# Kernel tuning notes

Measured on AMD Instinct MI355X. Metric: run time of the kernel, lower is better.

## Reference

```python
import jax, jax.numpy as jnp
import numpy as np

B, T, C = 2, 2048, 1024
H, D = 16, 64
F = 4096
EPS = 1e-5


def _layernorm(x, scale, shift):
    mean = jnp.mean(x, axis=-1, keepdims=True)
    var = jnp.mean((x - mean) ** 2, axis=-1, keepdims=True)  # unbiased=False
    return scale * (x - mean) * jax.lax.rsqrt(var + EPS) + shift


def setup_inputs() -> dict:
    key = jax.random.key(0)
    ks = jax.random.split(key, 16)
    s = lambda k, shape, fan_in: jax.random.normal(k, shape, jnp.float32) * (1.0 / np.sqrt(fan_in))
    return {
        "x": jax.random.normal(ks[0], (B, T, C), jnp.float32),
        # weights stored [in, out] so y = x @ W + b (same math as torch Linear)
        "Wq": s(ks[1], (C, H * D), C), "bq": jnp.zeros((H * D,), jnp.float32),
        "Wk": s(ks[2], (C, H * D), C), "bk": jnp.zeros((H * D,), jnp.float32),
        "Wv": s(ks[3], (C, H * D), C), "bv": jnp.zeros((H * D,), jnp.float32),
        "Wo": s(ks[4], (H * D, C), H * D), "bo": jnp.zeros((C,), jnp.float32),
        "W1": s(ks[5], (C, F), C), "b1": jnp.zeros((F,), jnp.float32),
        "W2": s(ks[6], (F, C), F), "b2": jnp.zeros((C,), jnp.float32),
        "ln1_scale": jnp.ones((C,), jnp.float32), "ln1_shift": jnp.zeros((C,), jnp.float32),
        "ln2_scale": jnp.ones((C,), jnp.float32), "ln2_shift": jnp.zeros((C,), jnp.float32),
    }


def reference(x, Wq, bq, Wk, bk, Wv, bv, Wo, bo, W1, b1, W2, b2,
              ln1_scale, ln1_shift, ln2_scale, ln2_shift):
    b, t, c = x.shape
    # --- attention sub-block ---
    h = _layernorm(x, ln1_scale, ln1_shift)
    q = (h @ Wq + bq).reshape(b, t, H, D)
    k = (h @ Wk + bk).reshape(b, t, H, D)
    v = (h @ Wv + bv).reshape(b, t, H, D)
    scores = jnp.einsum('bqhd,bkhd->bhqk', q, k)  # [B,H,T,T]
    causal = jnp.tril(jnp.ones((t, t), dtype=bool))
    scores = jnp.where(causal, scores, -jnp.inf)
    attn = jax.nn.softmax(scores / np.sqrt(D), axis=-1)
    ctx = jnp.einsum('bhqk,bkhd->bqhd', attn, v).reshape(b, t, H * D)
    x = x + (ctx @ Wo + bo)  # drop_rate=0 -> dropout is identity
    # --- MLP sub-block ---
    h = _layernorm(x, ln2_scale, ln2_shift)
    h = jax.nn.gelu(h @ W1 + b1, approximate=False)
    x = x + (h @ W2 + b2)
    return x
```

## Files before the change

kernel.cpp:

```cpp
#include <hip/hip_runtime.h>
#include <hip/hip_bf16.h>
#include <stdint.h>

#define B_ 2
#define T_ 2048
#define C_ 1024
#define H_ 16
#define D_ 64
#define F_ 4096
#define M_ (B_*T_)

typedef unsigned short ushort_t;
typedef __attribute__((ext_vector_type(8))) short short8;
typedef __attribute__((ext_vector_type(4))) float f32x4;

__device__ __forceinline__ float bf2f(ushort_t u) {
    union { unsigned u; float f; } c; c.u = ((unsigned)u) << 16; return c.f;
}
__device__ __forceinline__ ushort_t f2bf(float f) {
    union { float f; unsigned u; } c; c.f = f;
    unsigned u = c.u;
    unsigned r = (u + 0x7FFFu + ((u >> 16) & 1u)) >> 16;
    return (ushort_t)r;
}

__device__ __forceinline__ float fexp2(float x) { return __builtin_amdgcn_exp2f(x); }

__device__ __forceinline__ void async16(void* lds, const void* g) {
    __builtin_amdgcn_global_load_lds(
        (const __attribute__((address_space(1))) unsigned int*)(uintptr_t)g,
        (__attribute__((address_space(3))) unsigned int*)(uintptr_t)lds,
        16, 0, 0);
}

__global__ __launch_bounds__(256) void transpose_all_k(
    const float* __restrict__ Wq, const float* __restrict__ Wk,
    const float* __restrict__ Wv, const float* __restrict__ Wo,
    const float* __restrict__ W1, const float* __restrict__ W2,
    ushort_t* __restrict__ oq, ushort_t* __restrict__ ok,
    ushort_t* __restrict__ ov, ushort_t* __restrict__ oo,
    ushort_t* __restrict__ o1, ushort_t* __restrict__ o2) {
    __shared__ ushort_t tile[32][33];
    int id = blockIdx.x;
    const float* in; ushort_t* out; int R, Cc, bx, by;
    if (id < 4096) {
        int w = id >> 10, loc = id & 1023;
        in  = w == 0 ? Wq : w == 1 ? Wk : w == 2 ? Wv : Wo;
        out = w == 0 ? oq : w == 1 ? ok : w == 2 ? ov : oo;
        R = 1024; Cc = 1024; bx = loc & 31; by = loc >> 5;
    } else if (id < 8192) {
        int loc = id - 4096; in = W1; out = o1; R = 1024; Cc = 4096;
        bx = loc & 127; by = loc >> 7;
    } else {
        int loc = id - 8192; in = W2; out = o2; R = 4096; Cc = 1024;
        bx = loc & 31; by = loc >> 5;
    }
    int tx = threadIdx.x, ty = threadIdx.y;
    int x = bx * 32 + tx;
    int y0 = by * 32;
#pragma unroll
    for (int i = 0; i < 32; i += 8)
        tile[ty + i][tx] = f2bf(in[(size_t)(y0 + ty + i) * Cc + x]);
    __syncthreads();
    int x2 = y0 + tx;
    int y2 = bx * 32;
#pragma unroll
    for (int i = 0; i < 32; i += 8)
        out[(size_t)(y2 + ty + i) * R + x2] = tile[tx][ty + i];
}

__global__ __launch_bounds__(256) void ln_kernel(const float* __restrict__ xin,
                                                 const float* __restrict__ scale_p,
                                                 const float* __restrict__ shift_p,
                                                 ushort_t* __restrict__ out) {
    int row = blockIdx.x, t = threadIdx.x;
    int wv = t >> 6, lane = t & 63;
    const float* xr = xin + (size_t)row * 1024 + t * 4;
    float4 v = *(const float4*)xr;
    float f[4] = {v.x, v.y, v.z, v.w};
    float s = f[0] + f[1] + f[2] + f[3];
    float q = f[0]*f[0] + f[1]*f[1] + f[2]*f[2] + f[3]*f[3];
#pragma unroll
    for (int off = 1; off < 64; off <<= 1) {
        s += __shfl_xor(s, off, 64);
        q += __shfl_xor(q, off, 64);
    }
    __shared__ float sh_s[4], sh_q[4];
    if (lane == 0) { sh_s[wv] = s; sh_q[wv] = q; }
    __syncthreads();
    float S = sh_s[0] + sh_s[1] + sh_s[2] + sh_s[3];
    float Q = sh_q[0] + sh_q[1] + sh_q[2] + sh_q[3];
    float mean = S * (1.0f / 1024.0f);
    float var = Q * (1.0f / 1024.0f) - mean * mean;
    float rstd = rsqrtf(var + 1e-5f);
    float4 scv = *(const float4*)(scale_p + t * 4);
    float4 shv = *(const float4*)(shift_p + t * 4);
    ushort4 o;
    o.x = f2bf((f[0] - mean) * rstd * scv.x + shv.x);
    o.y = f2bf((f[1] - mean) * rstd * scv.y + shv.y);
    o.z = f2bf((f[2] - mean) * rstd * scv.z + shv.z);
    o.w = f2bf((f[3] - mean) * rstd * scv.w + shv.w);
    *(ushort4*)(out + (size_t)row * 1024 + t * 4) = o;
}

template <int MT, int EPI>
__global__ __launch_bounds__(256) void gemm_bt(const ushort_t* __restrict__ A,
                                               const ushort_t* __restrict__ Bt,
                                               const float* __restrict__ b0,
                                               const float* __restrict__ b1,
                                               const float* __restrict__ b2,
                                               const float* __restrict__ res,
                                               void* __restrict__ out0,
                                               void* __restrict__ out1,
                                               void* __restrict__ out2,
                                               int M, int N, int K) {
    __shared__ ushort_t As[32 * MT * 32];
    __shared__ ushort_t Bs[128 * 32];
    const int t = threadIdx.x;
    const int wv = t >> 6, lane = t & 63, lo = lane & 15, hi = lane >> 4;
    const int wr = wv >> 1, wc = wv & 1;
    const int mb = blockIdx.y, nb = blockIdx.x;

    f32x4 acc[MT][4];
#pragma unroll
    for (int i = 0; i < MT; ++i)
#pragma unroll
        for (int j = 0; j < 4; ++j) acc[i][j] = (f32x4){0.f, 0.f, 0.f, 0.f};

    for (int k0 = 0; k0 < K; k0 += 32) {
#pragma unroll
        for (int i = 0; i < MT / 2; ++i) {
            int c = i * 256 + t;
            int row = c >> 2, kc = c & 3;
            async16((char*)As + (size_t)(i * 256 + wv * 64) * 16,
                    A + (size_t)(mb * 32 * MT + row) * K + k0 + kc * 8);
        }
#pragma unroll
        for (int i = 0; i < 2; ++i) {
            int c = i * 256 + t;
            int row = c >> 2, kc = c & 3;
            async16((char*)Bs + (size_t)(i * 256 + wv * 64) * 16,
                    Bt + (size_t)(nb * 128 + row) * K + k0 + kc * 8);
        }
        __syncthreads();

        short8 af[MT], bfr[4];
#pragma unroll
        for (int mi = 0; mi < MT; ++mi)
            af[mi] = *(const short8*)(As + (wr * 16 * MT + mi * 16 + lo) * 32 + hi * 8);
#pragma unroll
        for (int ni = 0; ni < 4; ++ni)
            bfr[ni] = *(const short8*)(Bs + (wc * 64 + ni * 16 + lo) * 32 + hi * 8);
#pragma unroll
        for (int mi = 0; mi < MT; ++mi)
#pragma unroll
            for (int ni = 0; ni < 4; ++ni)
                acc[mi][ni] = __builtin_amdgcn_mfma_f32_16x16x32_bf16(
                    af[mi], bfr[ni], acc[mi][ni], 0, 0, 0);
        __syncthreads();
    }

#pragma unroll
    for (int ni = 0; ni < 4; ++ni) {
        int n = nb * 128 + wc * 64 + ni * 16 + lo;
        float bn;
        ushort_t* obf = nullptr;
        int coln = n, seg = 0;
        if (EPI == 3) {
            seg = n >> 10; coln = n & 1023;
            bn = (seg == 0 ? b0 : seg == 1 ? b1 : b2)[coln];
            obf = (ushort_t*)(seg == 0 ? out0 : out1);
        } else {
            bn = b0[n];
        }
#pragma unroll
        for (int mi = 0; mi < MT; ++mi) {
            if (EPI == 3 && seg == 2) {
                int m0 = mb * 32 * MT + wr * 16 * MT + mi * 16 + 4 * hi;
                ushort4 pk;
                pk.x = f2bf(acc[mi][ni][0] + bn);
                pk.y = f2bf(acc[mi][ni][1] + bn);
                pk.z = f2bf(acc[mi][ni][2] + bn);
                pk.w = f2bf(acc[mi][ni][3] + bn);
                *(ushort4*)((ushort_t*)out2 + (size_t)coln * M + m0) = pk;
            } else {
#pragma unroll
                for (int r = 0; r < 4; ++r) {
                    int m = mb * 32 * MT + wr * 16 * MT + mi * 16 + 4 * hi + r;
                    float v = acc[mi][ni][r] + bn;
                    if (EPI == 1) {
                        size_t idx = (size_t)m * N + n;
                        ((float*)out0)[idx] = v + res[idx];
                    } else if (EPI == 2) {
                        v = 0.5f * v * (1.0f + erff(v * 0.70710678118654752f));
                        ((ushort_t*)out0)[(size_t)m * N + n] = f2bf(v);
                    } else {
                        obf[(size_t)m * 1024 + coln] = f2bf(v);
                    }
                }
            }
        }
    }
}

__global__ __launch_bounds__(256) void attn_kernel(const ushort_t* __restrict__ q,
                                                   const ushort_t* __restrict__ k,
                                                   const ushort_t* __restrict__ vt,
                                                   ushort_t* __restrict__ ctx) {
    __shared__ ushort_t Ks[2][64 * 64];
    __shared__ ushort_t VTs[2][64 * 64];
    __shared__ ushort_t Ps[8][16 * 72];

    const int t = threadIdx.x;
    const int wv = t >> 6, lane = t & 63, lo = lane & 15, hi = lane >> 4;
    const int id = blockIdx.x;
    const int s = id >> 5;
    const int qb = (s < 8) ? s : 23 - s;
    const int bh = id & 31, b = bh >> 4, h = bh & 15;
    const int q0 = qb * 128;
    const size_t headoff = (size_t)h * 64;
    const size_t rowbase = (size_t)b * T_ * 1024;
    const ushort_t* vbase = vt + headoff * (size_t)M_ + (size_t)b * T_;

    short8 qf[2][2];
#pragma unroll
    for (int g = 0; g < 2; ++g) {
        const ushort_t* qp = q + rowbase + (size_t)(q0 + g * 64 + wv * 16 + lo) * 1024 + headoff;
        qf[g][0] = *(const short8*)(qp + hi * 8);
        qf[g][1] = *(const short8*)(qp + 32 + hi * 8);
    }

    float m_g[2], l_g[2];
    f32x4 o_acc[2][4];
#pragma unroll
    for (int g = 0; g < 2; ++g) {
        m_g[g] = -1e30f; l_g[g] = 0.f;
#pragma unroll
        for (int dt = 0; dt < 4; ++dt) o_acc[g][dt] = (f32x4){0.f, 0.f, 0.f, 0.f};
    }

    const int ktmax = 2 * qb + 1;
    const float SC = 0.18033688011112042f;
    const f32x4 NEG4 = (f32x4){-1e30f, -1e30f, -1e30f, -1e30f};

    auto stage = [&](int bb, int kt) {
        const int k0s = kt * 64;
#pragma unroll
        for (int i = 0; i < 2; ++i) {
            int c = i * 256 + t;
            int row = c >> 3, c8 = c & 7;
            int gsw = c8 ^ (row & 7);
            async16((char*)&Ks[bb][0] + (size_t)(i * 256 + wv * 64) * 16,
                    k + rowbase + (size_t)(k0s + row) * 1024 + headoff + gsw * 8);
            async16((char*)&VTs[bb][0] + (size_t)(i * 256 + wv * 64) * 16,
                    vbase + (size_t)row * M_ + k0s + gsw * 8);
        }
    };

    auto softmax_g = [&](f32x4* sacc, int gi) {
        float mx = -1e30f;
#pragma unroll
        for (int kt16 = 0; kt16 < 4; ++kt16)
#pragma unroll
            for (int r = 0; r < 4; ++r) mx = fmaxf(mx, sacc[kt16][r]);
        mx = fmaxf(mx, __shfl_xor(mx, 16, 64));
        mx = fmaxf(mx, __shfl_xor(mx, 32, 64));
        float mnew = fmaxf(m_g[gi], mx);
        float alpha = fexp2(m_g[gi] - mnew);
        m_g[gi] = mnew;
        ushort_t* Pw = Ps[wv * 2 + gi];
        float rs = 0.f;
#pragma unroll
        for (int kt16 = 0; kt16 < 4; ++kt16) {
#pragma unroll
            for (int r = 0; r < 4; ++r) {
                float p = fexp2(sacc[kt16][r] - mnew);
                rs += p;
                Pw[lo * 72 + kt16 * 16 + 4 * hi + r] = f2bf(p);
            }
        }
        rs += __shfl_xor(rs, 16, 64);
        rs += __shfl_xor(rs, 32, 64);
        l_g[gi] = l_g[gi] * alpha + rs;
#pragma unroll
        for (int r = 0; r < 4; ++r) {
            float ab = __shfl(alpha, 4 * hi + r, 64);
#pragma unroll
            for (int dt = 0; dt < 4; ++dt) o_acc[gi][dt][r] *= ab;
        }
    };

    stage(0, 0);
    for (int kt = 0; kt <= ktmax; ++kt) {
        const int bb = kt & 1;
        const int k0 = kt * 64;
        __syncthreads();
        if (kt < ktmax) stage(bb ^ 1, kt + 1);

        short8 pf[2][2];
        int any_g[2];
#pragma unroll
        for (int g = 0; g < 2; ++g) {
            const int qg0 = q0 + g * 64 + wv * 16;
            const int diff = qg0 - k0;
            any_g[g] = (diff >= 0);
            if (!any_g[g]) continue;
            const int cmax = diff >= 48 ? 3 : (diff >> 4);

            f32x4 sacc[4];
#pragma unroll
            for (int kt16 = 0; kt16 < 4; ++kt16) {
                if (kt16 <= cmax) {
                    int row = kt16 * 16 + lo, sw = row & 7;
                    short8 kf0 = *(const short8*)(&Ks[bb][0] + row * 64 + (hi ^ sw) * 8);
                    short8 kf1 = *(const short8*)(&Ks[bb][0] + row * 64 + ((4 + hi) ^ sw) * 8);
                    f32x4 z = (f32x4){0.f, 0.f, 0.f, 0.f};
                    z = __builtin_amdgcn_mfma_f32_16x16x32_bf16(kf0, qf[g][0], z, 0, 0, 0);
                    z = __builtin_amdgcn_mfma_f32_16x16x32_bf16(kf1, qf[g][1], z, 0, 0, 0);
#pragma unroll
                    for (int r = 0; r < 4; ++r) sacc[kt16][r] = z[r] * SC;
                } else {
                    sacc[kt16] = NEG4;
                }
            }
            if (diff < 64) {
                const int qrow = diff + lo;
#pragma unroll
                for (int r = 0; r < 4; ++r) {
                    int key = cmax * 16 + 4 * hi + r;
                    if (key > qrow) sacc[cmax][r] = -1e30f;
                }
            }

            softmax_g(sacc, g);

            pf[g][0] = *(const short8*)(Ps[wv * 2 + g] + lo * 72 + hi * 8);
            pf[g][1] = *(const short8*)(Ps[wv * 2 + g] + lo * 72 + 32 + hi * 8);
        }

#pragma unroll
        for (int dt = 0; dt < 4; ++dt) {
            int row = dt * 16 + lo, sw = row & 7;
            short8 vf0 = *(const short8*)(&VTs[bb][0] + row * 64 + (hi ^ sw) * 8);
            short8 vf1 = *(const short8*)(&VTs[bb][0] + row * 64 + ((4 + hi) ^ sw) * 8);
#pragma unroll
            for (int g = 0; g < 2; ++g) {
                if (!any_g[g]) continue;
                o_acc[g][dt] = __builtin_amdgcn_mfma_f32_16x16x32_bf16(pf[g][0], vf0, o_acc[g][dt], 0, 0, 0);
                o_acc[g][dt] = __builtin_amdgcn_mfma_f32_16x16x32_bf16(pf[g][1], vf1, o_acc[g][dt], 0, 0, 0);
            }
        }
    }

#pragma unroll
    for (int g = 0; g < 2; ++g) {
#pragma unroll
        for (int r = 0; r < 4; ++r) {
            float lb = __shfl(l_g[g], 4 * hi + r, 64);
            float inv = 1.0f / lb;
            size_t row = rowbase + (size_t)(q0 + g * 64 + wv * 16 + 4 * hi + r) * 1024 + headoff;
#pragma unroll
            for (int dt = 0; dt < 4; ++dt)
                ctx[row + dt * 16 + lo] = f2bf(o_acc[g][dt][r] * inv);
        }
    }
}

extern "C" void kernel_launch(void* const* d_in, const int* in_sizes, int n_in,
                              void* d_out, int out_size, void* d_ws, size_t ws_size,
                              hipStream_t stream) {
    (void)in_sizes; (void)n_in; (void)out_size; (void)ws_size;
    const float* x    = (const float*)d_in[0];
    const float* Wq   = (const float*)d_in[1];
    const float* bq   = (const float*)d_in[2];
    const float* Wk   = (const float*)d_in[3];
    const float* bk   = (const float*)d_in[4];
    const float* Wv   = (const float*)d_in[5];
    const float* bv   = (const float*)d_in[6];
    const float* Wo   = (const float*)d_in[7];
    const float* bo   = (const float*)d_in[8];
    const float* W1   = (const float*)d_in[9];
    const float* b1   = (const float*)d_in[10];
    const float* W2   = (const float*)d_in[11];
    const float* b2   = (const float*)d_in[12];
    const float* ln1s = (const float*)d_in[13];
    const float* ln1b = (const float*)d_in[14];
    const float* ln2s = (const float*)d_in[15];
    const float* ln2b = (const float*)d_in[16];

    char* ws = (char*)d_ws;
    const size_t MB = 1024 * 1024;
    ushort_t* wqkv = (ushort_t*)(ws + 0 * MB);
    ushort_t* wtq  = (ushort_t*)(ws + 0 * MB);
    ushort_t* wtk  = (ushort_t*)(ws + 2 * MB);
    ushort_t* wtv  = (ushort_t*)(ws + 4 * MB);
    ushort_t* wto  = (ushort_t*)(ws + 6 * MB);
    ushort_t* wt1  = (ushort_t*)(ws + 8 * MB);
    ushort_t* wt2  = (ushort_t*)(ws + 16 * MB);
    ushort_t* hbuf = (ushort_t*)(ws + 24 * MB);
    ushort_t* qb_  = (ushort_t*)(ws + 32 * MB);
    ushort_t* kb_  = (ushort_t*)(ws + 40 * MB);
    ushort_t* ctx  = (ushort_t*)(ws + 56 * MB);
    ushort_t* hid  = (ushort_t*)(ws + 32 * MB);
    float*    x1   = (float*)(ws + 64 * MB);
    ushort_t* vtb  = (ushort_t*)(ws + 64 * MB);

    transpose_all_k<<<12288, dim3(32, 8), 0, stream>>>(Wq, Wk, Wv, Wo, W1, W2,
                                                       wtq, wtk, wtv, wto, wt1, wt2);

    ln_kernel<<<4096, 256, 0, stream>>>(x, ln1s, ln1b, hbuf);

    gemm_bt<4, 3><<<dim3(24, 32), 256, 0, stream>>>(hbuf, wqkv, bq, bk, bv, nullptr,
                                                    qb_, kb_, vtb, 4096, 3072, 1024);

    attn_kernel<<<512, 256, 0, stream>>>(qb_, kb_, vtb, ctx);

    gemm_bt<2, 1><<<dim3(8, 64), 256, 0, stream>>>(ctx, wto, bo, nullptr, nullptr, x,
                                                   x1, nullptr, nullptr, 4096, 1024, 1024);

    ln_kernel<<<4096, 256, 0, stream>>>(x1, ln2s, ln2b, hbuf);

    gemm_bt<4, 2><<<dim3(32, 32), 256, 0, stream>>>(hbuf, wt1, b1, nullptr, nullptr, nullptr,
                                                    hid, nullptr, nullptr, 4096, 4096, 1024);

    gemm_bt<2, 1><<<dim3(8, 64), 256, 0, stream>>>(hid, wt2, b2, nullptr, nullptr, x1,
                                                   (float*)d_out, nullptr, nullptr, 4096, 1024, 4096);
}
```

Baseline: 431.6 us.

## Stage GEMM epilogues through LDS for coalesced bf16 stores; keep residual in bf16

GEMM epilogues for the QKV, FC1 and Wo projections now write bf16 results into shared memory with an XOR swizzle. They then store them as 16-byte row-contiguous vectors instead of scattered 2-byte stores. The intermediate residual x1 is stored as bf16 instead of fp32, and the second LayerNorm and the final GEMM epilogue read it in bf16, which halves that traffic. This adds extra syncs and LDS round trips, and rounding the residual stream to bf16 costs some precision.

```diff
diff --git a/kernel.cpp b/kernel.cpp
--- a/kernel.cpp
+++ b/kernel.cpp
@@ -69,15 +69,21 @@
         out[(size_t)(y2 + ty + i) * R + x2] = tile[tx][ty + i];
 }
 
-__global__ __launch_bounds__(256) void ln_kernel(const float* __restrict__ xin,
+template <int INBF>
+__global__ __launch_bounds__(256) void ln_kernel(const void* __restrict__ xin,
                                                  const float* __restrict__ scale_p,
                                                  const float* __restrict__ shift_p,
                                                  ushort_t* __restrict__ out) {
     int row = blockIdx.x, t = threadIdx.x;
     int wv = t >> 6, lane = t & 63;
-    const float* xr = xin + (size_t)row * 1024 + t * 4;
-    float4 v = *(const float4*)xr;
-    float f[4] = {v.x, v.y, v.z, v.w};
+    float f[4];
+    if (INBF) {
+        ushort4 v = *(const ushort4*)((const ushort_t*)xin + (size_t)row * 1024 + t * 4);
+        f[0] = bf2f(v.x); f[1] = bf2f(v.y); f[2] = bf2f(v.z); f[3] = bf2f(v.w);
+    } else {
+        float4 v = *(const float4*)((const float*)xin + (size_t)row * 1024 + t * 4);
+        f[0] = v.x; f[1] = v.y; f[2] = v.z; f[3] = v.w;
+    }
     float s = f[0] + f[1] + f[2] + f[3];
     float q = f[0]*f[0] + f[1]*f[1] + f[2]*f[2] + f[3]*f[3];
 #pragma unroll
@@ -109,13 +115,14 @@
                                                const float* __restrict__ b0,
                                                const float* __restrict__ b1,
                                                const float* __restrict__ b2,
-                                               const float* __restrict__ res,
+                                               const void* __restrict__ res,
                                                void* __restrict__ out0,
                                                void* __restrict__ out1,
                                                void* __restrict__ out2,
                                                int M, int N, int K) {
-    __shared__ ushort_t As[32 * MT * 32];
-    __shared__ ushort_t Bs[128 * 32];
+    __shared__ ushort_t smem[32 * MT * 32 + 128 * 32];
+    ushort_t* As = smem;
+    ushort_t* Bs = smem + 32 * MT * 32;
     const int t = threadIdx.x;
     const int wv = t >> 6, lane = t & 63, lo = lane & 15, hi = lane >> 4;
     const int wr = wv >> 1, wc = wv & 1;
@@ -160,22 +167,27 @@
         __syncthreads();
     }
 
-#pragma unroll
-    for (int ni = 0; ni < 4; ++ni) {
-        int n = nb * 128 + wc * 64 + ni * 16 + lo;
-        float bn;
-        ushort_t* obf = nullptr;
-        int coln = n, seg = 0;
-        if (EPI == 3) {
-            seg = n >> 10; coln = n & 1023;
-            bn = (seg == 0 ? b0 : seg == 1 ? b1 : b2)[coln];
-            obf = (ushort_t*)(seg == 0 ? out0 : out1);
-        } else {
-            bn = b0[n];
-        }
-#pragma unroll
-        for (int mi = 0; mi < MT; ++mi) {
-            if (EPI == 3 && seg == 2) {
+    if (EPI == 5) {
+#pragma unroll
+        for (int ni = 0; ni < 4; ++ni) {
+            int n = nb * 128 + wc * 64 + ni * 16 + lo;
+            float bn = b0[n];
+#pragma unroll
+            for (int mi = 0; mi < MT; ++mi)
+#pragma unroll
+                for (int r = 0; r < 4; ++r) {
+                    int m = mb * 32 * MT + wr * 16 * MT + mi * 16 + 4 * hi + r;
+                    size_t idx = (size_t)m * N + n;
+                    ((float*)out0)[idx] = acc[mi][ni][r] + bn + bf2f(((const ushort_t*)res)[idx]);
+                }
+        }
+    } else if (EPI == 3 && nb >= 16) {
+#pragma unroll
+        for (int ni = 0; ni < 4; ++ni) {
+            int coln = (nb & 7) * 128 + wc * 64 + ni * 16 + lo;
+            float bn = b2[coln];
+#pragma unroll
+            for (int mi = 0; mi < MT; ++mi) {
                 int m0 = mb * 32 * MT + wr * 16 * MT + mi * 16 + 4 * hi;
                 ushort4 pk;
                 pk.x = f2bf(acc[mi][ni][0] + bn);
@@ -183,21 +195,51 @@
                 pk.z = f2bf(acc[mi][ni][2] + bn);
                 pk.w = f2bf(acc[mi][ni][3] + bn);
                 *(ushort4*)((ushort_t*)out2 + (size_t)coln * M + m0) = pk;
-            } else {
-#pragma unroll
-                for (int r = 0; r < 4; ++r) {
-                    int m = mb * 32 * MT + wr * 16 * MT + mi * 16 + 4 * hi + r;
-                    float v = acc[mi][ni][r] + bn;
-                    if (EPI == 1) {
-                        size_t idx = (size_t)m * N + n;
-                        ((float*)out0)[idx] = v + res[idx];
-                    } else if (EPI == 2) {
-                        v = 0.5f * v * (1.0f + erff(v * 0.70710678118654752f));
-                        ((ushort_t*)out0)[(size_t)m * N + n] = f2bf(v);
-                    } else {
-                        obf[(size_t)m * 1024 + coln] = f2bf(v);
+            }
+        }
+    } else {
+        const float* bptr; ushort_t* obase; int colbase, ostride;
+        if (EPI == 3) {
+            int sg = nb >> 3;
+            bptr = sg ? b1 : b0;
+            obase = (ushort_t*)(sg ? out1 : out0);
+            colbase = (nb & 7) * 128; ostride = 1024;
+        } else {
+            bptr = b0; obase = (ushort_t*)out0;
+            colbase = nb * 128; ostride = N;
+        }
+#pragma unroll
+        for (int p = 0; p < 2; ++p) {
+            __syncthreads();
+#pragma unroll
+            for (int e = 0; e < 2; ++e) {
+                int ni = 2 * p + e;
+                int ncol = colbase + wc * 64 + ni * 16 + lo;
+                float bn = bptr[ncol];
+#pragma unroll
+                for (int mi = 0; mi < MT; ++mi)
+#pragma unroll
+                    for (int r = 0; r < 4; ++r) {
+                        int ml = wr * 16 * MT + mi * 16 + 4 * hi + r;
+                        float v = acc[mi][ni][r] + bn;
+                        if (EPI == 2) v = 0.5f * v * (1.0f + erff(v * 0.70710678118654752f));
+                        if (EPI == 4) v += ((const float*)res)[(size_t)(mb * 32 * MT + ml) * ostride + ncol];
+                        int col = wc * 32 + e * 16 + lo;
+                        smem[ml * 64 + (col ^ ((((unsigned)ml >> 2) & 3) << 4))] = f2bf(v);
                     }
-                }
+            }
+            __syncthreads();
+            const int tpr = 8 / MT;
+            int row = t / tpr, sub = t % tpr;
+            int cstart = sub * 8 * MT;
+            int half = cstart >> 5;
+            int nst = colbase + 32 * p + 64 * half + (cstart - 32 * half);
+            ushort_t* dst = obase + (size_t)(mb * 32 * MT + row) * ostride + nst;
+#pragma unroll
+            for (int j = 0; j < MT; ++j) {
+                int c = cstart + 8 * j;
+                int csw = c ^ ((((unsigned)row >> 2) & 3) << 4);
+                *(short8*)(dst + 8 * j) = *(const short8*)(smem + row * 64 + csw);
             }
         }
     }
@@ -402,27 +444,27 @@
     ushort_t* kb_  = (ushort_t*)(ws + 40 * MB);
     ushort_t* ctx  = (ushort_t*)(ws + 56 * MB);
     ushort_t* hid  = (ushort_t*)(ws + 32 * MB);
-    float*    x1   = (float*)(ws + 64 * MB);
     ushort_t* vtb  = (ushort_t*)(ws + 64 * MB);
+    ushort_t* x1b  = (ushort_t*)(ws + 64 * MB);
 
     transpose_all_k<<<12288, dim3(32, 8), 0, stream>>>(Wq, Wk, Wv, Wo, W1, W2,
                                                        wtq, wtk, wtv, wto, wt1, wt2);
 
-    ln_kernel<<<4096, 256, 0, stream>>>(x, ln1s, ln1b, hbuf);
+    ln_kernel<0><<<4096, 256, 0, stream>>>(x, ln1s, ln1b, hbuf);
 
     gemm_bt<4, 3><<<dim3(24, 32), 256, 0, stream>>>(hbuf, wqkv, bq, bk, bv, nullptr,
                                                     qb_, kb_, vtb, 4096, 3072, 1024);
 
     attn_kernel<<<512, 256, 0, stream>>>(qb_, kb_, vtb, ctx);
 
-    gemm_bt<2, 1><<<dim3(8, 64), 256, 0, stream>>>(ctx, wto, bo, nullptr, nullptr, x,
-                                                   x1, nullptr, nullptr, 4096, 1024, 1024);
-
-    ln_kernel<<<4096, 256, 0, stream>>>(x1, ln2s, ln2b, hbuf);
+    gemm_bt<2, 4><<<dim3(8, 64), 256, 0, stream>>>(ctx, wto, bo, nullptr, nullptr, x,
+                                                   x1b, nullptr, nullptr, 4096, 1024, 1024);
+
+    ln_kernel<1><<<4096, 256, 0, stream>>>(x1b, ln2s, ln2b, hbuf);
 
     gemm_bt<4, 2><<<dim3(32, 32), 256, 0, stream>>>(hbuf, wt1, b1, nullptr, nullptr, nullptr,
                                                     hid, nullptr, nullptr, 4096, 4096, 1024);
 
-    gemm_bt<2, 1><<<dim3(8, 64), 256, 0, stream>>>(hid, wt2, b2, nullptr, nullptr, x1,
+    gemm_bt<2, 5><<<dim3(8, 64), 256, 0, stream>>>(hid, wt2, b2, nullptr, nullptr, x1b,
                                                    (float*)d_out, nullptr, nullptr, 4096, 1024, 4096);
 }
```

After: 447.9 us. +3.8%, slower.
